# Optimization experiments

Measured on AMD Instinct MI355X. Metric: run time of the kernel, lower is better.

Reference implementation:

```python
import jax, jax.numpy as jnp
import numpy as np

B = 32768      # number of voxels (batch)
P = 32         # points per voxel (point_num)
IN = 7         # input feature dim
D2 = 64        # output_dim // 2


def setup_inputs() -> dict:
    key = jax.random.key(0)
    k1, k2, k3 = jax.random.split(key, 3)
    x = jax.random.normal(k1, (B, P, IN), dtype=jnp.float32)
    W = jax.random.normal(k2, (D2, IN), dtype=jnp.float32) * (1.0 / np.sqrt(IN))
    b = jax.random.normal(k3, (D2,), dtype=jnp.float32) * 0.01
    return {"x": x, "W": W, "b": b}


def reference(x, W, b):
    batch, pnum, _ = x.shape
    d2 = W.shape[0]
    out_dim = 2 * d2
    # Linear on flattened points: [B*P, IN] @ [IN, D2] + b -> [B, P, D2]
    local_f = (jnp.einsum("bpi,di->bpd", x, W) + b)  # [B, P, D2]
    # Faithful to torch: view (NOT transpose) local_f as [B, D2, P], max over last axis
    global_f = jnp.max(local_f.reshape(batch, d2, pnum), axis=-1)  # [B, D2]
    # Per-point concat of local and (broadcast) global features -> [B, P, 2*D2]
    element_f = jnp.concatenate(
        [local_f, jnp.broadcast_to(global_f[:, None, :], (batch, pnum, d2))],
        axis=-1,
    )
    # Faithful final view (reshape, not transpose): [B, 2*D2, P]
    return element_f.reshape(batch, out_dim, pnum)
```

## Files before the change

kernel.cpp:

```cpp
#include <hip/hip_runtime.h>


#define B_VOX 32768
#define P_PTS 32
#define IN_F  7
#define D2_F  64

__global__ __launch_bounds__(256) void vfe_kernel(
    const float* __restrict__ x,
    const float* __restrict__ W,
    const float* __restrict__ bias,
    float* __restrict__ out)
{
    __shared__ alignas(16) float sxp[P_PTS * 8];
    __shared__ alignas(16) float slds[P_PTS * D2_F + D2_F];

    const int t    = threadIdx.x;
    const int b    = blockIdx.x;
    const int lane = t & 63;
    const int wv   = t >> 6;

    const float* xb = x + (size_t)b * (P_PTS * IN_F);
    if (t < P_PTS * IN_F) {
        const int p = t / IN_F;
        const int k = t - p * IN_F;
        sxp[p * 8 + k] = xb[t];
    }

    const float* Wr = W + lane * IN_F;
    const float w0 = Wr[0], w1 = Wr[1], w2 = Wr[2], w3 = Wr[3];
    const float w4 = Wr[4], w5 = Wr[5], w6 = Wr[6];
    const float bl = bias[lane];

    __syncthreads();

    const int half = lane >> 5;

    #pragma unroll
    for (int s = 0; s < 8; ++s) {
        const int p = 8 * wv + s;
        const float4 lo = *(const float4*)&sxp[p * 8];
        const float4 hi = *(const float4*)&sxp[p * 8 + 4];
        float acc = bl;
        acc = fmaf(lo.x, w0, acc);
        acc = fmaf(lo.y, w1, acc);
        acc = fmaf(lo.z, w2, acc);
        acc = fmaf(lo.w, w3, acc);
        acc = fmaf(hi.x, w4, acc);
        acc = fmaf(hi.y, w5, acc);
        acc = fmaf(hi.z, w6, acc);
        slds[p * D2_F + lane] = acc;

        float m = acc;
        m = fmaxf(m, __shfl_xor(m, 16, 64));
        m = fmaxf(m, __shfl_xor(m,  8, 64));
        m = fmaxf(m, __shfl_xor(m,  4, 64));
        m = fmaxf(m, __shfl_xor(m,  2, 64));
        m = fmaxf(m, __shfl_xor(m,  1, 64));
        if ((lane & 31) == 0)
            slds[2048 + 16 * wv + 2 * s + half] = m;
    }
    __syncthreads();

    float4* out4 = (float4*)(out + (size_t)b * (P_PTS * 2 * D2_F));
    #pragma unroll
    for (int s = 0; s < 4; ++s) {
        const int idx = t + 256 * s;
        const int o   = 4 * idx;
        const int c   = o & 127;
        const int p   = o >> 7;
        const int a   = (c < 64) ? (p * 64 + c) : (2048 + (c - 64));
        const float4 v = *(const float4*)&slds[a];
        out4[idx] = v;
    }
}

extern "C" void kernel_launch(void* const* d_in, const int* in_sizes, int n_in,
                              void* d_out, int out_size, void* d_ws, size_t ws_size,
                              hipStream_t stream) {
    const float* x    = (const float*)d_in[0];
    const float* W    = (const float*)d_in[1];
    const float* bias = (const float*)d_in[2];
    float* out        = (float*)d_out;

    vfe_kernel<<<B_VOX, 256, 0, stream>>>(x, W, bias, out);
}
```

Before: 550.5 us.

## Remap threads to point-by-channel-group and write local features directly

Each thread now owns one point and eight output channels, split as two groups of four, and loads its own x row straight from global memory. The x staging in LDS and the full local-feature staging buffer are removed. Local features are written to the output as float4 stores from registers, and only the 64 group maxima pass through a small LDS array. This cuts LDS traffic and one barrier, but each thread holds 56 weight registers and does scalar strided loads of x.

```diff
diff --git a/kernel.cpp b/kernel.cpp
--- a/kernel.cpp
+++ b/kernel.cpp
@@ -2,9 +2,13 @@
 
 
 #define B_VOX 32768
-#define P_PTS 32
-#define IN_F  7
-#define D2_F  64
+
+__device__ __forceinline__ float group8_max(float v) {
+    v = fmaxf(v, __shfl_xor(v, 1, 8));
+    v = fmaxf(v, __shfl_xor(v, 2, 8));
+    v = fmaxf(v, __shfl_xor(v, 4, 8));
+    return v;
+}
 
 __global__ __launch_bounds__(256) void vfe_kernel(
     const float* __restrict__ x,
@@ -12,67 +16,71 @@
     const float* __restrict__ bias,
     float* __restrict__ out)
 {
-    __shared__ alignas(16) float sxp[P_PTS * 8];
-    __shared__ alignas(16) float slds[P_PTS * D2_F + D2_F];
+    __shared__ alignas(16) float sg[64];
 
-    const int t    = threadIdx.x;
-    const int b    = blockIdx.x;
-    const int lane = t & 63;
-    const int wv   = t >> 6;
+    const int t = threadIdx.x;
+    const int b = blockIdx.x;
+    const int p = t >> 3;
+    const int g = t & 7;
 
-    const float* xb = x + (size_t)b * (P_PTS * IN_F);
-    if (t < P_PTS * IN_F) {
-        const int p = t / IN_F;
-        const int k = t - p * IN_F;
-        sxp[p * 8 + k] = xb[t];
+    const float* xr = x + (size_t)b * 224 + p * 7;
+    const float x0 = xr[0], x1 = xr[1], x2 = xr[2], x3 = xr[3];
+    const float x4 = xr[4], x5 = xr[5], x6 = xr[6];
+
+    const float4* Wlo = (const float4*)(W + 28 * g);
+    const float4* Whi = (const float4*)(W + 224 + 28 * g);
+    float wl[28], wh[28];
+    #pragma unroll
+    for (int q = 0; q < 7; ++q) {
+        const float4 a = Wlo[q];
+        wl[4*q+0] = a.x; wl[4*q+1] = a.y; wl[4*q+2] = a.z; wl[4*q+3] = a.w;
+        const float4 c = Whi[q];
+        wh[4*q+0] = c.x; wh[4*q+1] = c.y; wh[4*q+2] = c.z; wh[4*q+3] = c.w;
+    }
+    const float4 blo = *(const float4*)(bias + 4 * g);
+    const float4 bhi = *(const float4*)(bias + 32 + 4 * g);
+    const float bl[4] = {blo.x, blo.y, blo.z, blo.w};
+    const float bh[4] = {bhi.x, bhi.y, bhi.z, bhi.w};
+
+    float accLo[4], accHi[4];
+    #pragma unroll
+    for (int j = 0; j < 4; ++j) {
+        float a = bl[j];
+        a = fmaf(x0, wl[7*j+0], a);
+        a = fmaf(x1, wl[7*j+1], a);
+        a = fmaf(x2, wl[7*j+2], a);
+        a = fmaf(x3, wl[7*j+3], a);
+        a = fmaf(x4, wl[7*j+4], a);
+        a = fmaf(x5, wl[7*j+5], a);
+        a = fmaf(x6, wl[7*j+6], a);
+        accLo[j] = a;
+        float c = bh[j];
+        c = fmaf(x0, wh[7*j+0], c);
+        c = fmaf(x1, wh[7*j+1], c);
+        c = fmaf(x2, wh[7*j+2], c);
+        c = fmaf(x3, wh[7*j+3], c);
+        c = fmaf(x4, wh[7*j+4], c);
+        c = fmaf(x5, wh[7*j+5], c);
+        c = fmaf(x6, wh[7*j+6], c);
+        accHi[j] = c;
     }
 
-    const float* Wr = W + lane * IN_F;
-    const float w0 = Wr[0], w1 = Wr[1], w2 = Wr[2], w3 = Wr[3];
-    const float w4 = Wr[4], w5 = Wr[5], w6 = Wr[6];
-    const float bl = bias[lane];
+    float* ob = out + (size_t)b * 4096;
+    *(float4*)(ob + p * 128 + 4 * g)      = make_float4(accLo[0], accLo[1], accLo[2], accLo[3]);
+    *(float4*)(ob + p * 128 + 32 + 4 * g) = make_float4(accHi[0], accHi[1], accHi[2], accHi[3]);
+
+    float mLo = group8_max(fmaxf(fmaxf(accLo[0], accLo[1]), fmaxf(accLo[2], accLo[3])));
+    float mHi = group8_max(fmaxf(fmaxf(accHi[0], accHi[1]), fmaxf(accHi[2], accHi[3])));
+    if (g == 0)
+        *(float2*)&sg[2 * p] = make_float2(mLo, mHi);
 
     __syncthreads();
 
-    const int half = lane >> 5;
-
-    #pragma unroll
-    for (int s = 0; s < 8; ++s) {
-        const int p = 8 * wv + s;
-        const float4 lo = *(const float4*)&sxp[p * 8];
-        const float4 hi = *(const float4*)&sxp[p * 8 + 4];
-        float acc = bl;
-        acc = fmaf(lo.x, w0, acc);
-        acc = fmaf(lo.y, w1, acc);
-        acc = fmaf(lo.z, w2, acc);
-        acc = fmaf(lo.w, w3, acc);
-        acc = fmaf(hi.x, w4, acc);
-        acc = fmaf(hi.y, w5, acc);
-        acc = fmaf(hi.z, w6, acc);
-        slds[p * D2_F + lane] = acc;
-
-        float m = acc;
-        m = fmaxf(m, __shfl_xor(m, 16, 64));
-        m = fmaxf(m, __shfl_xor(m,  8, 64));
-        m = fmaxf(m, __shfl_xor(m,  4, 64));
-        m = fmaxf(m, __shfl_xor(m,  2, 64));
-        m = fmaxf(m, __shfl_xor(m,  1, 64));
-        if ((lane & 31) == 0)
-            slds[2048 + 16 * wv + 2 * s + half] = m;
-    }
-    __syncthreads();
-
-    float4* out4 = (float4*)(out + (size_t)b * (P_PTS * 2 * D2_F));
-    #pragma unroll
-    for (int s = 0; s < 4; ++s) {
-        const int idx = t + 256 * s;
-        const int o   = 4 * idx;
-        const int c   = o & 127;
-        const int p   = o >> 7;
-        const int a   = (c < 64) ? (p * 64 + c) : (2048 + (c - 64));
-        const float4 v = *(const float4*)&slds[a];
-        out4[idx] = v;
-    }
+    const int j4 = t & 15;
+    const int p0 = t >> 4;
+    const float4 g4 = *(const float4*)&sg[4 * j4];
+    *(float4*)(ob + p0 * 128 + 64 + 4 * j4)        = g4;
+    *(float4*)(ob + (p0 + 16) * 128 + 64 + 4 * j4) = g4;
 }
 
 extern "C" void kernel_launch(void* const* d_in, const int* in_sizes, int n_in,
```

After: 627.5 us. +14.0%, slower.
